# Kernel optimization log

Hardware: AMD Instinct MI355X
Metric: run time of the kernel (lower is better)

## Reference

```python
import jax, jax.numpy as jnp
import numpy as np

L, S, N, E = 1024, 1024, 16, 1024

def setup_inputs() -> dict:
    key = jax.random.key(0)
    ks = jax.random.split(key, 7)
    return {
        "query": jax.random.normal(ks[0], (L, N, E), dtype=jnp.float32),
        "key": jax.random.normal(ks[1], (S, N, E), dtype=jnp.float32),
        "value": jax.random.normal(ks[2], (S, N, E), dtype=jnp.float32),
        "q_proj_weight": jax.random.normal(ks[3], (E, E), dtype=jnp.float32) * (E ** -0.5),
        "k_proj_weight": jax.random.normal(ks[4], (E, E), dtype=jnp.float32) * (E ** -0.5),
        "v_proj_weight": jax.random.normal(ks[5], (E, E), dtype=jnp.float32) * (E ** -0.5),
        "in_proj_bias": jax.random.normal(ks[6], (3 * E,), dtype=jnp.float32) * 0.02,
    }

def reference(query, key, value, q_proj_weight, k_proj_weight, v_proj_weight, in_proj_bias):
    # query: (L, N, E); key/value: (S, N, E); single head => head_dim = E
    e = query.shape[-1]
    scaling = jnp.asarray(e, query.dtype) ** -0.5
    # F.linear(x, W, b) = x @ W.T + b
    q = (jnp.einsum("lne,fe->lnf", query, q_proj_weight) + in_proj_bias[:e]) * scaling
    k = jnp.einsum("sne,fe->snf", key, k_proj_weight) + in_proj_bias[e:2 * e]
    v = jnp.einsum("sne,fe->snf", value, v_proj_weight) + in_proj_bias[2 * e:]
    # scores: (N, L, S)
    scores = jnp.einsum("lne,sne->nls", q, k)
    attn = jax.nn.softmax(scores, axis=-1)
    # output back to (L, N, E)
    out = jnp.einsum("nls,sne->lne", attn, v)
    return out
```

## Files before the change

kernel.cpp:

```cpp
#include <hip/hip_runtime.h>
#include <stdint.h>


typedef __attribute__((ext_vector_type(8))) short bf16x8;
typedef __attribute__((ext_vector_type(4))) float f32x4;

__device__ __forceinline__ float bf2f(unsigned short u) {
    union { unsigned int i; float f; } w; w.i = ((unsigned int)u) << 16; return w.f;
}
__device__ __forceinline__ unsigned short f2bf(float f) {
    union { float f; unsigned int i; } w; w.f = f;
    unsigned int r = (w.i + 0x7FFFu + ((w.i >> 16) & 1u)) >> 16;
    return (unsigned short)r;
}

__device__ __forceinline__ void g2l16(const unsigned short* g, unsigned short* l) {
    __builtin_amdgcn_global_load_lds(
        (const __attribute__((address_space(1))) unsigned int*)g,
        (__attribute__((address_space(3))) unsigned int*)l, 16, 0, 0);
}

#define BM 256
#define BN 256
#define BK 32

template <int BIAS_MODE, typename OutT>
__global__ __launch_bounds__(512, 2) void gemm_bt2(
    const unsigned short* __restrict__ A,
    const unsigned short* __restrict__ B,
    OutT* __restrict__ C,
    const float* __restrict__ bias,
    float scale, int K,
    long lda, long ldb, long ldc,
    long aBatch, long bBatch, long cBatch,
    int gridM, int gridN)
{
    __shared__ __align__(16) unsigned short lds[65536];

    const int tid  = threadIdx.x;
    const int wave = tid >> 6;
    const int lane = tid & 63;
    const int lr   = lane & 15;
    const int q4   = lane >> 4;
    const int wm   = wave >> 2;
    const int wn   = wave & 3;

    const int per  = gridM * gridN;
    const int bid  = blockIdx.x;
    const int bz   = bid / per;
    const int rem  = bid - bz * per;
    const int brow = rem % gridM;
    const int bcol = rem / gridM;
    const long m0 = (long)brow * BM;
    const long n0 = (long)bcol * BN;
    A += (long)bz * aBatch;
    B += (long)bz * bBatch;
    C += (long)bz * cBatch;

    const int tswz  = tid ^ ((tid >> 3) & 7);
    const int srow  = tswz >> 2;
    const int skoff = (tswz & 3) * 8;
    const unsigned short* aS0 = A + (m0 + srow) * lda + skoff;
    const unsigned short* aS1 = A + (m0 + 128 + srow) * lda + skoff;
    const unsigned short* bS0 = B + (n0 + srow) * ldb + skoff;
    const unsigned short* bS1 = B + (n0 + 128 + srow) * ldb + skoff;
    const int ldsW = wave * 512;

    const int myoff = (((lr << 2) | q4) ^ ((lr >> 1) & 7)) << 3;

    f32x4 acc[8][4];
    const f32x4 zero = {0.f, 0.f, 0.f, 0.f};
#pragma unroll
    for (int m = 0; m < 8; m++)
#pragma unroll
        for (int n = 0; n < 4; n++) acc[m][n] = zero;

    const int nkt = K / BK;

#pragma unroll
    for (int t = 0; t < 3; t++) {
        const long kb = (long)t * BK;
        unsigned short* base = &lds[t * 16384];
        g2l16(aS0 + kb, base + ldsW);
        g2l16(aS1 + kb, base + 4096 + ldsW);
        g2l16(bS0 + kb, base + 8192 + ldsW);
        g2l16(bS1 + kb, base + 12288 + ldsW);
    }
    asm volatile("s_waitcnt vmcnt(8)" ::: "memory");
    __builtin_amdgcn_s_barrier();

    for (int kt = 0; kt < nkt; kt++) {
        const int buf  = kt & 3;
        const int sbuf = (kt + 3) & 3;
        const int st   = (kt + 3 < nkt) ? kt + 3 : nkt - 1;
        const long kb  = (long)st * BK;
        const unsigned short* At = &lds[buf * 16384];
        const unsigned short* Bt = At + 8192;
        unsigned short* sb = &lds[sbuf * 16384];

        bf16x8 af[4], bfr[4];
#pragma unroll
        for (int m = 0; m < 4; m++)
            af[m] = *(const bf16x8*)&At[(wm * 128 + m * 16) * 32 + myoff];
#pragma unroll
        for (int n = 0; n < 4; n++)
            bfr[n] = *(const bf16x8*)&Bt[(wn * 64 + n * 16) * 32 + myoff];
        g2l16(aS0 + kb, sb + ldsW);
        g2l16(aS1 + kb, sb + 4096 + ldsW);
        __builtin_amdgcn_s_barrier();
        __builtin_amdgcn_s_setprio(1);
#pragma unroll
        for (int m = 0; m < 4; m++)
#pragma unroll
            for (int n = 0; n < 4; n++)
                acc[m][n] = __builtin_amdgcn_mfma_f32_16x16x32_bf16(
                    af[m], bfr[n], acc[m][n], 0, 0, 0);
        __builtin_amdgcn_s_setprio(0);
        __builtin_amdgcn_s_barrier();

        bf16x8 ag[4];
#pragma unroll
        for (int m = 0; m < 4; m++)
            ag[m] = *(const bf16x8*)&At[(wm * 128 + 64 + m * 16) * 32 + myoff];
        g2l16(bS0 + kb, sb + 8192 + ldsW);
        g2l16(bS1 + kb, sb + 12288 + ldsW);
        __builtin_amdgcn_s_barrier();
        __builtin_amdgcn_s_setprio(1);
#pragma unroll
        for (int m = 0; m < 4; m++)
#pragma unroll
            for (int n = 0; n < 4; n++)
                acc[4 + m][n] = __builtin_amdgcn_mfma_f32_16x16x32_bf16(
                    ag[m], bfr[n], acc[4 + m][n], 0, 0, 0);
        __builtin_amdgcn_s_setprio(0);
        asm volatile("s_waitcnt vmcnt(8)" ::: "memory");
        __builtin_amdgcn_s_barrier();
        __builtin_amdgcn_sched_barrier(0);
    }

#pragma unroll
    for (int n = 0; n < 4; n++) {
        const long col = n0 + wn * 64 + n * 16 + lr;
        float cb = 0.f;
        if constexpr (BIAS_MODE == 1) cb = bias[col];
#pragma unroll
        for (int m = 0; m < 8; m++) {
            const long row = m0 + wm * 128 + m * 16 + q4 * 4;
#pragma unroll
            for (int r = 0; r < 4; r++) {
                float v = acc[m][n][r];
                if constexpr (BIAS_MODE == 1) v += cb;
                if constexpr (BIAS_MODE == 2) v += bias[row + r];
                v *= scale;
                if constexpr (sizeof(OutT) == 2)
                    C[(row + r) * ldc + col] = (OutT)f2bf(v);
                else
                    C[(row + r) * ldc + col] = v;
            }
        }
    }
}

__global__ __launch_bounds__(256) void cvt_f32_bf16(
    const float* __restrict__ in, unsigned short* __restrict__ out, long n8)
{
    const long stride = (long)gridDim.x * blockDim.x;
    for (long i = (long)blockIdx.x * blockDim.x + threadIdx.x; i < n8; i += stride) {
        const float4* p = (const float4*)(in + i * 8);
        float4 a = p[0], b = p[1];
        bf16x8 v;
        v[0] = (short)f2bf(a.x); v[1] = (short)f2bf(a.y);
        v[2] = (short)f2bf(a.z); v[3] = (short)f2bf(a.w);
        v[4] = (short)f2bf(b.x); v[5] = (short)f2bf(b.y);
        v[6] = (short)f2bf(b.z); v[7] = (short)f2bf(b.w);
        *(bf16x8*)(out + i * 8) = v;
    }
}

__global__ __launch_bounds__(256) void softmax_rows(unsigned short* __restrict__ base)
{
    unsigned short* p = base + (long)blockIdx.x * 1024;
    const int tid = threadIdx.x;
    ushort4 u = ((const ushort4*)p)[tid];
    float x0 = bf2f(u.x), x1 = bf2f(u.y), x2 = bf2f(u.z), x3 = bf2f(u.w);
    x0 = fminf(fmaxf(x0, -1e30f), 1e30f);
    x1 = fminf(fmaxf(x1, -1e30f), 1e30f);
    x2 = fminf(fmaxf(x2, -1e30f), 1e30f);
    x3 = fminf(fmaxf(x3, -1e30f), 1e30f);

    float m = fmaxf(fmaxf(x0, x1), fmaxf(x2, x3));
#pragma unroll
    for (int o = 32; o > 0; o >>= 1) m = fmaxf(m, __shfl_xor(m, o));
    __shared__ float redm[4], reds[4];
    const int wave = tid >> 6, lane = tid & 63;
    if (lane == 0) redm[wave] = m;
    __syncthreads();
    m = fmaxf(fmaxf(redm[0], redm[1]), fmaxf(redm[2], redm[3]));

    float e0 = __expf(x0 - m), e1 = __expf(x1 - m);
    float e2 = __expf(x2 - m), e3 = __expf(x3 - m);
    float s = e0 + e1 + e2 + e3;
#pragma unroll
    for (int o = 32; o > 0; o >>= 1) s += __shfl_xor(s, o);
    if (lane == 0) reds[wave] = s;
    __syncthreads();
    s = reds[0] + reds[1] + reds[2] + reds[3];
    const float inv = 1.0f / s;

    ushort4 ov = make_ushort4(f2bf(e0 * inv), f2bf(e1 * inv),
                              f2bf(e2 * inv), f2bf(e3 * inv));
    ((ushort4*)p)[tid] = ov;
}

extern "C" void kernel_launch(void* const* d_in, const int* in_sizes, int n_in,
                              void* d_out, int out_size, void* d_ws, size_t ws_size,
                              hipStream_t stream) {
    const float* query = (const float*)d_in[0];
    const float* keyp  = (const float*)d_in[1];
    const float* valp  = (const float*)d_in[2];
    const float* wq    = (const float*)d_in[3];
    const float* wk    = (const float*)d_in[4];
    const float* wv    = (const float*)d_in[5];
    const float* bias  = (const float*)d_in[6];
    float* out = (float*)d_out;

    unsigned short* WSA = (unsigned short*)d_ws;
    unsigned short* WSB = WSA + 16777216;
    unsigned short* OC  = (unsigned short*)d_out;
    unsigned short* OD  = OC + 16777216;

    const dim3 cblk(256, 1, 1);
    const dim3 gblk(512, 1, 1);

    cvt_f32_bf16<<<2048, cblk, 0, stream>>>(query, WSA, 2097152);
    cvt_f32_bf16<<<512, cblk, 0, stream>>>(wq, WSB, 131072);
    gemm_bt2<1, unsigned short><<<256, gblk, 0, stream>>>(
        WSA, WSB, OC, bias, 0.03125f, 1024,
        1024, 1024, 1024, 0, 0, 0, 64, 4);
    cvt_f32_bf16<<<2048, cblk, 0, stream>>>(keyp, WSA, 2097152);
    cvt_f32_bf16<<<512, cblk, 0, stream>>>(wk, WSB, 131072);
    gemm_bt2<1, unsigned short><<<256, gblk, 0, stream>>>(
        WSA, WSB, OD, bias + 1024, 1.0f, 1024,
        1024, 1024, 1024, 0, 0, 0, 64, 4);
    gemm_bt2<0, unsigned short><<<256, gblk, 0, stream>>>(
        OC, OD, WSB, nullptr, 1.0f, 1024,
        16384, 16384, 1024, 1024, 1024, 1048576, 4, 4);
    softmax_rows<<<16384, cblk, 0, stream>>>(WSB);
    cvt_f32_bf16<<<2048, cblk, 0, stream>>>(valp, OC, 2097152);
    cvt_f32_bf16<<<512, cblk, 0, stream>>>(wv, OD, 131072);
    gemm_bt2<2, unsigned short><<<256, gblk, 0, stream>>>(
        OD, OC, WSA, bias + 2048, 1.0f, 1024,
        1024, 16384, 1024, 0, 1024, 1048576, 4, 4);
    gemm_bt2<0, float><<<256, gblk, 0, stream>>>(
        WSB, WSA, out, nullptr, 1.0f, 1024,
        1024, 1024, 16384, 1048576, 1048576, 1024, 4, 4);
}
```

Baseline: 482.1 us.

## Stage GEMM epilogue through LDS, remap block order, merge conversion launches

The GEMM epilogue now writes accumulators into swizzled shared memory and then emits 16-byte coalesced global stores, replacing scattered 2- or 4-byte per-lane stores. Block indices are permuted (p&7)<<5 | p>>3 so that consecutive blocks are spread across XCDs while tiles sharing operands stay on the same XCD's L2. The paired input/weight float-to-bf16 conversions are merged into one launch each. The risks are extra barriers and LDS traffic in the epilogue, and the block mapping, which hardcodes a 256-block grid.

```diff
diff --git a/kernel.cpp b/kernel.cpp
--- a/kernel.cpp
+++ b/kernel.cpp
@@ -45,12 +45,13 @@
     const int wm   = wave >> 2;
     const int wn   = wave & 3;
 
-    const int per  = gridM * gridN;
-    const int bid  = blockIdx.x;
-    const int bz   = bid / per;
-    const int rem  = bid - bz * per;
-    const int brow = rem % gridM;
-    const int bcol = rem / gridM;
+    const int p    = blockIdx.x;
+    const int l    = ((p & 7) << 5) + (p >> 3);
+    const int bcol = l % gridN;
+    const int t2   = l / gridN;
+    const int brow = t2 % gridM;
+    const int bz   = t2 / gridM;
+
     const long m0 = (long)brow * BM;
     const long n0 = (long)bcol * BN;
     A += (long)bz * aBatch;
@@ -138,42 +139,89 @@
         __builtin_amdgcn_sched_barrier(0);
     }
 
-#pragma unroll
-    for (int n = 0; n < 4; n++) {
-        const long col = n0 + wn * 64 + n * 16 + lr;
-        float cb = 0.f;
-        if constexpr (BIAS_MODE == 1) cb = bias[col];
-#pragma unroll
-        for (int m = 0; m < 8; m++) {
-            const long row = m0 + wm * 128 + m * 16 + q4 * 4;
-#pragma unroll
-            for (int r = 0; r < 4; r++) {
-                float v = acc[m][n][r];
-                if constexpr (BIAS_MODE == 1) v += cb;
-                if constexpr (BIAS_MODE == 2) v += bias[row + r];
-                v *= scale;
-                if constexpr (sizeof(OutT) == 2)
-                    C[(row + r) * ldc + col] = (OutT)f2bf(v);
-                else
-                    C[(row + r) * ldc + col] = v;
+    asm volatile("s_waitcnt vmcnt(0)" ::: "memory");
+    __syncthreads();
+
+    if constexpr (sizeof(OutT) == 2) {
+#pragma unroll
+        for (int m = 0; m < 8; m++)
+#pragma unroll
+            for (int n = 0; n < 4; n++) {
+                const int col = wn * 64 + n * 16 + lr;
+#pragma unroll
+                for (int r = 0; r < 4; r++) {
+                    const int row = wm * 128 + m * 16 + q4 * 4 + r;
+                    float v = acc[m][n][r];
+                    if constexpr (BIAS_MODE == 1) v += bias[n0 + col];
+                    if constexpr (BIAS_MODE == 2) v += bias[m0 + row];
+                    v *= scale;
+                    lds[row * 256 + (col ^ (((row >> 2) & 3) << 4))] = f2bf(v);
+                }
+            }
+        __syncthreads();
+#pragma unroll
+        for (int i = 0; i < 16; i++) {
+            const int g   = i * 512 + tid;
+            const int row = g >> 5;
+            const int ch  = g & 31;
+            bf16x8 v = *(const bf16x8*)&lds[row * 256 + ((ch * 8) ^ (((row >> 2) & 3) << 4))];
+            *(bf16x8*)((unsigned short*)C + (m0 + row) * ldc + n0 + ch * 8) = v;
+        }
+    } else {
+        float* fl = (float*)lds;
+#pragma unroll
+        for (int h = 0; h < 2; h++) {
+            __syncthreads();
+            if (wm == h) {
+#pragma unroll
+                for (int m = 0; m < 8; m++)
+#pragma unroll
+                    for (int n = 0; n < 4; n++) {
+                        const int col = wn * 64 + n * 16 + lr;
+#pragma unroll
+                        for (int r = 0; r < 4; r++) {
+                            const int rowh = m * 16 + q4 * 4 + r;
+                            float v = acc[m][n][r];
+                            if constexpr (BIAS_MODE == 1) v += bias[n0 + col];
+                            if constexpr (BIAS_MODE == 2) v += bias[m0 + h * 128 + rowh];
+                            v *= scale;
+                            fl[rowh * 256 + (col ^ (((rowh >> 2) & 3) << 4))] = v;
+                        }
+                    }
+            }
+            __syncthreads();
+#pragma unroll
+            for (int i = 0; i < 16; i++) {
+                const int g   = i * 512 + tid;
+                const int row = g >> 6;
+                const int ch  = g & 63;
+                float4 v = *(const float4*)&fl[row * 256 + ((ch * 4) ^ (((row >> 2) & 3) << 4))];
+                *(float4*)((float*)C + (m0 + h * 128 + row) * ldc + n0 + ch * 4) = v;
             }
         }
     }
 }
 
-__global__ __launch_bounds__(256) void cvt_f32_bf16(
-    const float* __restrict__ in, unsigned short* __restrict__ out, long n8)
+__global__ __launch_bounds__(256) void cvt2_f32_bf16(
+    const float* __restrict__ inA, unsigned short* __restrict__ outA, long n8A,
+    const float* __restrict__ inB, unsigned short* __restrict__ outB, long n8B)
 {
+    const long total  = n8A + n8B;
     const long stride = (long)gridDim.x * blockDim.x;
-    for (long i = (long)blockIdx.x * blockDim.x + threadIdx.x; i < n8; i += stride) {
-        const float4* p = (const float4*)(in + i * 8);
-        float4 a = p[0], b = p[1];
+    for (long i = (long)blockIdx.x * blockDim.x + threadIdx.x; i < total; i += stride) {
+        const float* src;
+        unsigned short* dst;
+        long j;
+        if (i < n8A) { src = inA; dst = outA; j = i; }
+        else         { src = inB; dst = outB; j = i - n8A; }
+        const float4* pp = (const float4*)(src + j * 8);
+        float4 a = pp[0], b = pp[1];
         bf16x8 v;
         v[0] = (short)f2bf(a.x); v[1] = (short)f2bf(a.y);
         v[2] = (short)f2bf(a.z); v[3] = (short)f2bf(a.w);
         v[4] = (short)f2bf(b.x); v[5] = (short)f2bf(b.y);
         v[6] = (short)f2bf(b.z); v[7] = (short)f2bf(b.w);
-        *(bf16x8*)(out + i * 8) = v;
+        *(bf16x8*)(dst + j * 8) = v;
     }
 }
 
@@ -232,13 +280,11 @@
     const dim3 cblk(256, 1, 1);
     const dim3 gblk(512, 1, 1);
 
-    cvt_f32_bf16<<<2048, cblk, 0, stream>>>(query, WSA, 2097152);
-    cvt_f32_bf16<<<512, cblk, 0, stream>>>(wq, WSB, 131072);
+    cvt2_f32_bf16<<<2048, cblk, 0, stream>>>(query, WSA, 2097152, wq, WSB, 131072);
     gemm_bt2<1, unsigned short><<<256, gblk, 0, stream>>>(
         WSA, WSB, OC, bias, 0.03125f, 1024,
         1024, 1024, 1024, 0, 0, 0, 64, 4);
-    cvt_f32_bf16<<<2048, cblk, 0, stream>>>(keyp, WSA, 2097152);
-    cvt_f32_bf16<<<512, cblk, 0, stream>>>(wk, WSB, 131072);
+    cvt2_f32_bf16<<<2048, cblk, 0, stream>>>(keyp, WSA, 2097152, wk, WSB, 131072);
     gemm_bt2<1, unsigned short><<<256, gblk, 0, stream>>>(
         WSA, WSB, OD, bias + 1024, 1.0f, 1024,
         1024, 1024, 1024, 0, 0, 0, 64, 4);
@@ -246,8 +292,7 @@
         OC, OD, WSB, nullptr, 1.0f, 1024,
         16384, 16384, 1024, 1024, 1024, 1048576, 4, 4);
     softmax_rows<<<16384, cblk, 0, stream>>>(WSB);
-    cvt_f32_bf16<<<2048, cblk, 0, stream>>>(valp, OC, 2097152);
-    cvt_f32_bf16<<<512, cblk, 0, stream>>>(wv, OD, 131072);
+    cvt2_f32_bf16<<<2048, cblk, 0, stream>>>(valp, OC, 2097152, wv, OD, 131072);
     gemm_bt2<2, unsigned short><<<256, gblk, 0, stream>>>(
         OD, OC, WSA, bias + 2048, 1.0f, 1024,
         1024, 16384, 1024, 0, 1024, 1048576, 4, 4);
```

Result: faster. 430.8 us (-10.6%).
